# Optimization experiments

Measured on AMD Instinct MI355X. Metric: run time of the kernel, lower is better.

The kernel has to match this reference:

```python
import jax, jax.numpy as jnp
import numpy as np

LAYER_SIZE = 8
STACK_SIZE = 2
RES_CH = 64
SKIP_CH = 128
N = 16
L = 8192
NUM_BLOCKS = LAYER_SIZE * STACK_SIZE


def _dilations():
    return [2 ** lev for _ in range(STACK_SIZE) for lev in range(LAYER_SIZE)]


def setup_inputs() -> dict:
    key = jax.random.key(0)
    k1, k2, k3, k4 = jax.random.split(key, 4)
    x = jax.random.normal(k1, (N, RES_CH, L), dtype=jnp.float32)
    # conv weights scaled ~1/sqrt(fan_in) to keep gates in a sane range
    W_dil = jax.random.normal(k2, (NUM_BLOCKS, RES_CH, RES_CH, 2), dtype=jnp.float32) * 0.088
    W_res = jax.random.normal(k3, (NUM_BLOCKS, RES_CH, RES_CH), dtype=jnp.float32) * 0.125
    W_skip = jax.random.normal(k4, (NUM_BLOCKS, SKIP_CH, RES_CH), dtype=jnp.float32) * 0.125
    return {"x": x, "W_dil": W_dil, "W_res": W_res, "W_skip": W_skip}


def reference(x, W_dil, W_res, W_skip):
    dilations = _dilations()
    out = x
    skips = []
    for i, d in enumerate(dilations):
        wd = W_dil[i]    # (Cout, Cin, 2)
        wr = W_res[i]    # (C, C) 1x1
        ws = W_skip[i]   # (S, C) 1x1
        # dilated causal conv, kernel_size=2, no padding -> length L-d
        y = (jnp.einsum('oi,nil->nol', wd[:, :, 0], out[:, :, :-d])
             + jnp.einsum('oi,nil->nol', wd[:, :, 1], out[:, :, d:]))
        # gated activation: tanh and sigmoid of the SAME dilated output
        g = jnp.tanh(y) * jax.nn.sigmoid(y)
        # NOTE: source has `if self.pooling > 1` with self.pooling a bool,
        # so AvgPool1d is never applied; pool_out == g always.
        res = jnp.einsum('oi,nil->nol', wr, g) + out[:, :, -g.shape[2]:]
        skips.append(jnp.einsum('oi,nil->nol', ws, g))
        out = res
    osize = out.shape[2]
    skip_out = skips[0][:, :, -osize:]
    for s in skips[1:]:
        skip_out = skip_out + s[:, :, -osize:]
    return (out, skip_out)
```

## Files before the change

### kernel.cpp

```cpp
#include <hip/hip_runtime.h>


#define NBATCH 16
#define C 64
#define SC 128
#define L0 8192
#define OSIZE 7682
#define TILE 64
#define ST 128

typedef __bf16 bf16x8 __attribute__((ext_vector_type(8)));
typedef __bf16 bf16x4 __attribute__((ext_vector_type(4)));
typedef float  f32x4  __attribute__((ext_vector_type(4)));

__global__ __launch_bounds__(256) void pack_weights(
    const float* __restrict__ Wd, const float* __restrict__ Wr,
    const float* __restrict__ Ws,
    __bf16* __restrict__ Wdm, __bf16* __restrict__ Wrm, __bf16* __restrict__ Wsm)
{
    int idx = blockIdx.x * 256 + threadIdx.x;
    if (idx < 131072) {
        int kp = idx & 127, o = (idx >> 7) & 63, ly = idx >> 13;
        int k = kp & 63, tap = kp >> 6;
        Wdm[idx] = (__bf16)Wd[(((ly * 64 + o) * 64 + k) << 1) + tap];
    } else if (idx < 196608) {
        int j = idx - 131072;
        Wrm[j] = (__bf16)Wr[j];
    } else if (idx < 327680) {
        int j = idx - 196608;
        Wsm[j] = (__bf16)Ws[j];
    }
}

__global__ __launch_bounds__(256, 2) void wavenet_epoch5(
    const float* __restrict__ src, int Lin,
    float* __restrict__ dst,
    const __bf16* __restrict__ Wdm,
    const __bf16* __restrict__ Wrm,
    __bf16* __restrict__ gst, size_t slotHW)
{
    __shared__ __bf16 sxp[8][112][8];
    __shared__ __bf16 sgp[8][96][8];

    const int Lf = Lin - 31;
    const int n  = blockIdx.y;
    const int o0 = blockIdx.x * 64;
    if (o0 >= Lf) return;

    const int t    = threadIdx.x;
    const int lane = t & 63;
    const int wv   = t >> 6;
    const int q    = lane >> 4;
    const int nn   = lane & 15;
    const int kgw  = 2 * wv + (q >> 1);
    const int hf4  = (q & 1) * 4;

    f32x4 xs[6];
    const float* base = src + (size_t)(n * C + wv * 16 + q * 4) * L0 + o0;
    #pragma unroll
    for (int nt = 0; nt < 6; ++nt) {
        int p = nt * 16 + nn;
        bool inb = (o0 + p) < Lin;
        #pragma unroll
        for (int r = 0; r < 4; ++r)
            xs[nt][r] = inb ? base[(size_t)r * L0 + p] : 0.f;
        bf16x4 v;
        #pragma unroll
        for (int r = 0; r < 4; ++r) v[r] = (__bf16)xs[nt][r];
        *(bf16x4*)(&sxp[0][0][0] + ((size_t)kgw * 112 + 16 + p) * 8 + hf4) = v;
    }
    {
        bf16x4 z = {(__bf16)0.f, (__bf16)0.f, (__bf16)0.f, (__bf16)0.f};
        *(bf16x4*)(&sxp[0][0][0] + ((size_t)kgw * 112 + nn) * 8 + hf4) = z;
    }
    __syncthreads();

    #pragma unroll 1
    for (int l = 0; l < 5; ++l) {
        const int d = 1 << l;

        const __bf16* aw = Wdm + ((size_t)l * 64 + wv * 16 + nn) * 128 + q * 8;
        bf16x8 aW0 = *(const bf16x8*)(aw);
        bf16x8 aW1 = *(const bf16x8*)(aw + 32);
        bf16x8 aW2 = *(const bf16x8*)(aw + 64);
        bf16x8 aW3 = *(const bf16x8*)(aw + 96);
        #pragma unroll
        for (int nt = 0; nt < 6; ++nt) {
            int p = nt * 16 + nn;
            f32x4 acc = {0.f, 0.f, 0.f, 0.f};
            acc = __builtin_amdgcn_mfma_f32_16x16x32_bf16(aW0,
                    *(const bf16x8*)(&sxp[0][0][0] + ((size_t)(q    ) * 112 + 16 + p - d) * 8), acc, 0, 0, 0);
            acc = __builtin_amdgcn_mfma_f32_16x16x32_bf16(aW1,
                    *(const bf16x8*)(&sxp[0][0][0] + ((size_t)(4 + q) * 112 + 16 + p - d) * 8), acc, 0, 0, 0);
            acc = __builtin_amdgcn_mfma_f32_16x16x32_bf16(aW2,
                    *(const bf16x8*)(&sxp[0][0][0] + ((size_t)(q    ) * 112 + 16 + p    ) * 8), acc, 0, 0, 0);
            acc = __builtin_amdgcn_mfma_f32_16x16x32_bf16(aW3,
                    *(const bf16x8*)(&sxp[0][0][0] + ((size_t)(4 + q) * 112 + 16 + p    ) * 8), acc, 0, 0, 0);
            bf16x4 gv;
            #pragma unroll
            for (int r = 0; r < 4; ++r) {
                float y = fminf(fmaxf(acc[r], -20.f), 20.f);
                float u = __expf(y);
                gv[r] = (__bf16)(u * (u - 1.f) / fmaf(u, u, 1.f));
            }
            *(bf16x4*)(&sgp[0][0][0] + ((size_t)kgw * 96 + p) * 8 + hf4) = gv;
        }
        __syncthreads();

        const __bf16* ar = Wrm + ((size_t)l * 64 + wv * 16 + nn) * 64 + q * 8;
        bf16x8 aR0 = *(const bf16x8*)ar;
        bf16x8 aR1 = *(const bf16x8*)(ar + 32);
        #pragma unroll
        for (int nt = 0; nt < 6; ++nt) {
            int p = nt * 16 + nn;
            bf16x8 b0 = *(const bf16x8*)(&sgp[0][0][0] + ((size_t)(q    ) * 96 + p) * 8);
            bf16x8 b1 = *(const bf16x8*)(&sgp[0][0][0] + ((size_t)(4 + q) * 96 + p) * 8);
            xs[nt] = __builtin_amdgcn_mfma_f32_16x16x32_bf16(aR1, b1,
                     __builtin_amdgcn_mfma_f32_16x16x32_bf16(aR0, b0, xs[nt], 0, 0, 0),
                     0, 0, 0);
            bf16x4 v;
            #pragma unroll
            for (int r = 0; r < 4; ++r) v[r] = (__bf16)xs[nt][r];
            *(bf16x4*)(&sxp[0][0][0] + ((size_t)kgw * 112 + 16 + p) * 8 + hf4) = v;
        }

        const int Dl = (2 << l) - 1;
        const int Ll = Lin - Dl;
        const int sb = Ll - OSIZE;
        __bf16* gsl = gst + (size_t)l * slotHW;
        for (int item = t; item < 8 * 64; item += 256) {
            int p  = 31 + (item & 63);
            int kg = item >> 6;
            int i  = o0 + p - Dl;
            if (i >= sb && i < Ll) {
                *(bf16x8*)(gsl + (((size_t)n * 8 + kg) * OSIZE + (i - sb)) * 8)
                    = *(const bf16x8*)(&sgp[0][0][0] + ((size_t)kg * 96 + p) * 8);
            }
        }
        __syncthreads();
    }

    #pragma unroll
    for (int nt = 1; nt < 6; ++nt) {
        int p = nt * 16 + nn;
        if (p >= 31 && p < 95) {
            int i = o0 + p - 31;
            if (i < Lf) {
                #pragma unroll
                for (int r = 0; r < 4; ++r)
                    dst[(size_t)(n * C + wv * 16 + q * 4 + r) * L0 + i] = xs[nt][r];
            }
        }
    }
}

__global__ __launch_bounds__(256) void wavenet_layer_mfma(
    const float* __restrict__ src, int src_stride, int Lin,
    float* __restrict__ dst, int dst_stride,
    const __bf16* __restrict__ Wdm,
    const __bf16* __restrict__ Wrm,
    __bf16* __restrict__ gout,
    int d)
{
    extern __shared__ char smem_raw[];
    const int W    = TILE + d;
    const int Lout = Lin - d;
    const int n  = blockIdx.y;
    const int l0 = blockIdx.x * TILE;
    if (l0 >= Lout) return;
    const int np = min(TILE, Lout - l0);

    __bf16* sxp  = (__bf16*)smem_raw;
    float*  sres = (float*)(smem_raw + (size_t)8 * W * 8 * 2);
    __bf16* sgp  = (__bf16*)(sres + 64 * 65);

    const int t    = threadIdx.x;
    const int lane = t & 63;
    const int wv   = t >> 6;
    const int q    = lane >> 4;
    const int nn   = lane & 15;

    for (int item = t; item < 8 * W; item += 256) {
        int kg = item / W;
        int p  = item % W;
        bool inb = (l0 + p) < Lin;
        const float* col = src + (size_t)(n * C + kg * 8) * src_stride + l0 + p;
        float v[8];
        #pragma unroll
        for (int j = 0; j < 8; ++j) v[j] = inb ? col[(size_t)j * src_stride] : 0.f;
        bf16x8 bv;
        #pragma unroll
        for (int j = 0; j < 8; ++j) bv[j] = (__bf16)v[j];
        *(bf16x8*)(sxp + ((size_t)kg * W + p) * 8) = bv;
        int pr = p - d;
        if (pr >= 0 && pr < TILE) {
            #pragma unroll
            for (int j = 0; j < 8; ++j) sres[(kg * 8 + j) * 65 + pr] = v[j];
        }
    }
    __syncthreads();

    const __bf16* arow = Wdm + (size_t)(wv * 16 + nn) * 128 + q * 8;
    bf16x8 aW[4];
    #pragma unroll
    for (int ks = 0; ks < 4; ++ks) aW[ks] = *(const bf16x8*)(arow + ks * 32);

    #pragma unroll
    for (int nt = 0; nt < 4; ++nt) {
        int p0 = nt * 16;
        f32x4 acc = {0.f, 0.f, 0.f, 0.f};
        acc = __builtin_amdgcn_mfma_f32_16x16x32_bf16(aW[0],
                *(const bf16x8*)(sxp + ((size_t)(q    ) * W + p0 + nn    ) * 8), acc, 0, 0, 0);
        acc = __builtin_amdgcn_mfma_f32_16x16x32_bf16(aW[1],
                *(const bf16x8*)(sxp + ((size_t)(4 + q) * W + p0 + nn    ) * 8), acc, 0, 0, 0);
        acc = __builtin_amdgcn_mfma_f32_16x16x32_bf16(aW[2],
                *(const bf16x8*)(sxp + ((size_t)(q    ) * W + p0 + nn + d) * 8), acc, 0, 0, 0);
        acc = __builtin_amdgcn_mfma_f32_16x16x32_bf16(aW[3],
                *(const bf16x8*)(sxp + ((size_t)(4 + q) * W + p0 + nn + d) * 8), acc, 0, 0, 0);
        bf16x4 gv;
        #pragma unroll
        for (int r = 0; r < 4; ++r) {
            float y = fminf(fmaxf(acc[r], -20.f), 20.f);
            float u = __expf(y);
            gv[r] = (__bf16)(u * (u - 1.f) / fmaf(u, u, 1.f));
        }
        *(bf16x4*)(sgp + ((size_t)(2 * wv + (q >> 1)) * 64 + p0 + nn) * 8 + (q & 1) * 4) = gv;
    }
    __syncthreads();

    const __bf16* rrow = Wrm + (size_t)(wv * 16 + nn) * 64 + q * 8;
    bf16x8 aR0 = *(const bf16x8*)rrow;
    bf16x8 aR1 = *(const bf16x8*)(rrow + 32);
    #pragma unroll
    for (int nt = 0; nt < 4; ++nt) {
        int p0 = nt * 16;
        f32x4 acc = {0.f, 0.f, 0.f, 0.f};
        acc = __builtin_amdgcn_mfma_f32_16x16x32_bf16(aR0,
                *(const bf16x8*)(sgp + ((size_t)(q    ) * 64 + p0 + nn) * 8), acc, 0, 0, 0);
        acc = __builtin_amdgcn_mfma_f32_16x16x32_bf16(aR1,
                *(const bf16x8*)(sgp + ((size_t)(4 + q) * 64 + p0 + nn) * 8), acc, 0, 0, 0);
        if (p0 + nn < np) {
            #pragma unroll
            for (int r = 0; r < 4; ++r) {
                int ch = wv * 16 + q * 4 + r;
                dst[(size_t)(n * C + ch) * dst_stride + l0 + p0 + nn]
                    = acc[r] + sres[ch * 65 + p0 + nn];
            }
        }
    }

    const int sbase = Lout - OSIZE;
    for (int item = t; item < 8 * TILE; item += 256) {
        int p  = item & 63;
        int kg = item >> 6;
        int l  = l0 + p;
        if (l >= sbase && l < Lout) {
            *(bf16x8*)(gout + (((size_t)n * 8 + kg) * OSIZE + (l - sbase)) * 8)
                = *(const bf16x8*)(sgp + ((size_t)kg * 64 + p) * 8);
        }
    }
}

__global__ __launch_bounds__(256, 3) void skip_gemm(
    const __bf16* __restrict__ g,
    const __bf16* __restrict__ Wsm,
    float* __restrict__ skip,
    int G, int lybase, int init)
{
    __shared__ __bf16 Bb[3][8][ST][8];
    const int n  = blockIdx.y;
    const int l0 = blockIdx.x * ST;
    const int t  = threadIdx.x;
    const int lane = t & 63;
    const int wv   = __builtin_amdgcn_readfirstlane(t >> 6);
    const int q = lane >> 4, nn = lane & 15;

    f32x4 acc[2][8];
    #pragma unroll
    for (int mt = 0; mt < 2; ++mt)
        #pragma unroll
        for (int nt = 0; nt < 8; ++nt) acc[mt][nt] = (f32x4){0.f, 0.f, 0.f, 0.f};

    auto stage = [&](int buf, int gi) {
        const __bf16* gl = g + ((size_t)gi * NBATCH + n) * (size_t)8 * OSIZE * 8;
        #pragma unroll
        for (int j = 0; j < 4; ++j) {
            int kg   = 2 * wv + (j >> 1);
            int half = j & 1;
            const __bf16* srcp = gl + ((size_t)kg * OSIZE + l0 + half * 64) * 8
                                    + (size_t)lane * 8;
            __builtin_amdgcn_global_load_lds(
                (const __attribute__((address_space(1))) void*)srcp,
                (__attribute__((address_space(3))) void*)&Bb[buf][kg][half * 64][0],
                16, 0, 0);
        }
    };

    stage(0, 0);
    stage(1, G > 1 ? 1 : 0);

    for (int gi = 0; gi < G; ++gi) {
        const int cur = gi % 3;
        asm volatile("s_waitcnt vmcnt(4)" ::: "memory");
        __builtin_amdgcn_s_barrier();

        const __bf16* Wl = Wsm + (size_t)(lybase + gi) * SC * 64;
        bf16x8 a00 = *(const bf16x8*)(Wl + (size_t)(wv * 32 +      nn) * 64 +  0 + q * 8);
        bf16x8 a01 = *(const bf16x8*)(Wl + (size_t)(wv * 32 +      nn) * 64 + 32 + q * 8);
        bf16x8 a10 = *(const bf16x8*)(Wl + (size_t)(wv * 32 + 16 + nn) * 64 +  0 + q * 8);
        bf16x8 a11 = *(const bf16x8*)(Wl + (size_t)(wv * 32 + 16 + nn) * 64 + 32 + q * 8);
        __builtin_amdgcn_sched_barrier(0);

        stage((gi + 2) % 3, gi + 2 < G ? gi + 2 : G - 1);
        __builtin_amdgcn_sched_barrier(0);

        #pragma unroll
        for (int ks = 0; ks < 2; ++ks) {
            #pragma unroll
            for (int nt = 0; nt < 8; ++nt) {
                bf16x8 b = *(const bf16x8*)&Bb[cur][ks * 4 + q][nt * 16 + nn][0];
                acc[0][nt] = __builtin_amdgcn_mfma_f32_16x16x32_bf16(
                                 ks ? a01 : a00, b, acc[0][nt], 0, 0, 0);
                acc[1][nt] = __builtin_amdgcn_mfma_f32_16x16x32_bf16(
                                 ks ? a11 : a10, b, acc[1][nt], 0, 0, 0);
            }
        }
        __builtin_amdgcn_s_barrier();
    }

    #pragma unroll
    for (int mt = 0; mt < 2; ++mt)
        #pragma unroll
        for (int nt = 0; nt < 8; ++nt) {
            int p = l0 + nt * 16 + nn;
            if (p < OSIZE) {
                #pragma unroll
                for (int r = 0; r < 4; ++r) {
                    int s = wv * 32 + mt * 16 + q * 4 + r;
                    size_t idx = ((size_t)n * SC + s) * OSIZE + p;
                    float v = acc[mt][nt][r];
                    skip[idx] = init ? v : (skip[idx] + v);
                }
            }
        }
}

extern "C" void kernel_launch(void* const* d_in, const int* in_sizes, int n_in,
                              void* d_out, int out_size, void* d_ws, size_t ws_size,
                              hipStream_t stream) {
    const float* x      = (const float*)d_in[0];
    const float* W_dil  = (const float*)d_in[1];
    const float* W_res  = (const float*)d_in[2];
    const float* W_skip = (const float*)d_in[3];

    float* out  = (float*)d_out;
    float* skip = out + (size_t)NBATCH * C * OSIZE;

    float*  bufA = (float*)d_ws;
    float*  bufB = bufA + (size_t)NBATCH * C * L0;
    __bf16* Wdm  = (__bf16*)(bufB + (size_t)NBATCH * C * L0);
    __bf16* Wrm  = Wdm + 16 * 64 * 128;
    __bf16* Wsm  = Wrm + 16 * 64 * 64;
    __bf16* gst  = Wsm + 16 * 128 * 64;

    const size_t slotHW = (size_t)NBATCH * 8 * OSIZE * 8;
    const int G = 8;

    pack_weights<<<1280, 256, 0, stream>>>(W_dil, W_res, W_skip, Wdm, Wrm, Wsm);

    {
        int Lin = L0, Lf = Lin - 31;
        dim3 grid((Lf + 63) / 64, NBATCH);
        wavenet_epoch5<<<grid, 256, 0, stream>>>(
            x, Lin, bufA, Wdm, Wrm, gst, slotHW);
    }
    {
        const float* src = bufA; float* dsts[3] = {bufB, bufA, bufB};
        int Lin = L0 - 31;
        for (int k = 0; k < 3; ++k) {
            int i = 5 + k, d = 32 << k, Lout = Lin - d;
            int W = TILE + d;
            size_t smem = (size_t)128 * W + 64 * 65 * 4 + 8 * 64 * 8 * 2;
            dim3 grid((Lout + TILE - 1) / TILE, NBATCH);
            wavenet_layer_mfma<<<grid, 256, smem, stream>>>(
                src, L0, Lin, dsts[k], L0,
                Wdm + (size_t)i * 64 * 128, Wrm + (size_t)i * 64 * 64,
                gst + (size_t)(i % G) * slotHW, d);
            src = dsts[k]; Lin = Lout;
        }
    }
    {
        dim3 sgrid((OSIZE + ST - 1) / ST, NBATCH);
        skip_gemm<<<sgrid, 256, 0, stream>>>(gst, Wsm, skip, G, 0, 1);
    }

    {
        int Lin = L0 - 255;
        int Lf = Lin - 31;
        dim3 grid((Lf + 63) / 64, NBATCH);
        wavenet_epoch5<<<grid, 256, 0, stream>>>(
            bufB, Lin, bufA,
            Wdm + (size_t)8 * 64 * 128, Wrm + (size_t)8 * 64 * 64,
            gst, slotHW);
    }
    {
        const float* src = bufA;
        int Lin = L0 - 255 - 31;
        float* dsts[3] = {bufB, bufA, out};
        int strides[3] = {L0, L0, OSIZE};
        for (int k = 0; k < 3; ++k) {
            int i = 13 + k, d = 32 << k, Lout = Lin - d;
            int W = TILE + d;
            size_t smem = (size_t)128 * W + 64 * 65 * 4 + 8 * 64 * 8 * 2;
            dim3 grid((Lout + TILE - 1) / TILE, NBATCH);
            wavenet_layer_mfma<<<grid, 256, smem, stream>>>(
                src, L0, Lin, dsts[k], strides[k],
                Wdm + (size_t)i * 64 * 128, Wrm + (size_t)i * 64 * 64,
                gst + (size_t)(i % G) * slotHW, d);
            src = dsts[k]; Lin = Lout;
        }
    }
    {
        dim3 sgrid((OSIZE + ST - 1) / ST, NBATCH);
        skip_gemm<<<sgrid, 256, 0, stream>>>(gst, Wsm, skip, G, 8, 0);
    }
}
```

Measured before the change: 555.4 us.

## Halve skip GEMM tile width and double-buffer weight fragments in registers

```diff
diff --git a/kernel.cpp b/kernel.cpp
--- a/kernel.cpp
+++ b/kernel.cpp
@@ -7,7 +7,7 @@
 #define L0 8192
 #define OSIZE 7682
 #define TILE 64
-#define ST 128
+#define SST 64
 
 typedef __bf16 bf16x8 __attribute__((ext_vector_type(8)));
 typedef __bf16 bf16x4 __attribute__((ext_vector_type(4)));
@@ -261,77 +261,88 @@
     }
 }
 
-__global__ __launch_bounds__(256, 3) void skip_gemm(
+__global__ __launch_bounds__(256, 4) void skip_gemm(
     const __bf16* __restrict__ g,
     const __bf16* __restrict__ Wsm,
     float* __restrict__ skip,
     int G, int lybase, int init)
 {
-    __shared__ __bf16 Bb[3][8][ST][8];
+    __shared__ __bf16 Bb[3][8][SST][8];
     const int n  = blockIdx.y;
-    const int l0 = blockIdx.x * ST;
+    const int l0 = blockIdx.x * SST;
     const int t  = threadIdx.x;
     const int lane = t & 63;
     const int wv   = __builtin_amdgcn_readfirstlane(t >> 6);
     const int q = lane >> 4, nn = lane & 15;
 
-    f32x4 acc[2][8];
+    f32x4 acc[2][4];
     #pragma unroll
     for (int mt = 0; mt < 2; ++mt)
         #pragma unroll
-        for (int nt = 0; nt < 8; ++nt) acc[mt][nt] = (f32x4){0.f, 0.f, 0.f, 0.f};
+        for (int nt = 0; nt < 4; ++nt) acc[mt][nt] = (f32x4){0.f, 0.f, 0.f, 0.f};
 
     auto stage = [&](int buf, int gi) {
         const __bf16* gl = g + ((size_t)gi * NBATCH + n) * (size_t)8 * OSIZE * 8;
         #pragma unroll
-        for (int j = 0; j < 4; ++j) {
-            int kg   = 2 * wv + (j >> 1);
-            int half = j & 1;
-            const __bf16* srcp = gl + ((size_t)kg * OSIZE + l0 + half * 64) * 8
-                                    + (size_t)lane * 8;
+        for (int j = 0; j < 2; ++j) {
+            int kg = 2 * wv + j;
+            const __bf16* srcp = gl + ((size_t)kg * OSIZE + l0) * 8 + (size_t)lane * 8;
             __builtin_amdgcn_global_load_lds(
                 (const __attribute__((address_space(1))) void*)srcp,
-                (__attribute__((address_space(3))) void*)&Bb[buf][kg][half * 64][0],
+                (__attribute__((address_space(3))) void*)&Bb[buf][kg][0][0],
                 16, 0, 0);
         }
     };
-
+    auto loadA = [&](int gi, bf16x8* A) {
+        const __bf16* Wl = Wsm + (size_t)(lybase + gi) * SC * 64;
+        A[0] = *(const bf16x8*)(Wl + (size_t)(wv * 32 +      nn) * 64 +      q * 8);
+        A[1] = *(const bf16x8*)(Wl + (size_t)(wv * 32 +      nn) * 64 + 32 + q * 8);
+        A[2] = *(const bf16x8*)(Wl + (size_t)(wv * 32 + 16 + nn) * 64 +      q * 8);
+        A[3] = *(const bf16x8*)(Wl + (size_t)(wv * 32 + 16 + nn) * 64 + 32 + q * 8);
+    };
+    auto mfma16 = [&](const bf16x8* A, int cur) {
+        #pragma unroll
+        for (int ks = 0; ks < 2; ++ks) {
+            #pragma unroll
+            for (int nt = 0; nt < 4; ++nt) {
+                bf16x8 b = *(const bf16x8*)&Bb[cur][ks * 4 + q][nt * 16 + nn][0];
+                acc[0][nt] = __builtin_amdgcn_mfma_f32_16x16x32_bf16(
+                                 A[ks], b, acc[0][nt], 0, 0, 0);
+                acc[1][nt] = __builtin_amdgcn_mfma_f32_16x16x32_bf16(
+                                 A[2 + ks], b, acc[1][nt], 0, 0, 0);
+            }
+        }
+    };
+
+    bf16x8 aA[4], aB[4];
     stage(0, 0);
+    loadA(0, aA);
     stage(1, G > 1 ? 1 : 0);
 
-    for (int gi = 0; gi < G; ++gi) {
-        const int cur = gi % 3;
-        asm volatile("s_waitcnt vmcnt(4)" ::: "memory");
+    for (int gi = 0; gi < G; gi += 2) {
+        asm volatile("s_waitcnt vmcnt(6)" ::: "memory");
         __builtin_amdgcn_s_barrier();
-
-        const __bf16* Wl = Wsm + (size_t)(lybase + gi) * SC * 64;
-        bf16x8 a00 = *(const bf16x8*)(Wl + (size_t)(wv * 32 +      nn) * 64 +  0 + q * 8);
-        bf16x8 a01 = *(const bf16x8*)(Wl + (size_t)(wv * 32 +      nn) * 64 + 32 + q * 8);
-        bf16x8 a10 = *(const bf16x8*)(Wl + (size_t)(wv * 32 + 16 + nn) * 64 +  0 + q * 8);
-        bf16x8 a11 = *(const bf16x8*)(Wl + (size_t)(wv * 32 + 16 + nn) * 64 + 32 + q * 8);
         __builtin_amdgcn_sched_barrier(0);
-
+        loadA(gi + 1 < G ? gi + 1 : gi, aB);
         stage((gi + 2) % 3, gi + 2 < G ? gi + 2 : G - 1);
         __builtin_amdgcn_sched_barrier(0);
-
-        #pragma unroll
-        for (int ks = 0; ks < 2; ++ks) {
-            #pragma unroll
-            for (int nt = 0; nt < 8; ++nt) {
-                bf16x8 b = *(const bf16x8*)&Bb[cur][ks * 4 + q][nt * 16 + nn][0];
-                acc[0][nt] = __builtin_amdgcn_mfma_f32_16x16x32_bf16(
-                                 ks ? a01 : a00, b, acc[0][nt], 0, 0, 0);
-                acc[1][nt] = __builtin_amdgcn_mfma_f32_16x16x32_bf16(
-                                 ks ? a11 : a10, b, acc[1][nt], 0, 0, 0);
-            }
-        }
+        mfma16(aA, gi % 3);
         __builtin_amdgcn_s_barrier();
+
+        asm volatile("s_waitcnt vmcnt(6)" ::: "memory");
+        __builtin_amdgcn_s_barrier();
+        __builtin_amdgcn_sched_barrier(0);
+        loadA(gi + 2 < G ? gi + 2 : gi, aA);
+        stage((gi + 3) % 3, gi + 3 < G ? gi + 3 : G - 1);
+        __builtin_amdgcn_sched_barrier(0);
+        mfma16(aB, (gi + 1) % 3);
+        __builtin_amdgcn_s_barrier();
     }
 
     #pragma unroll
     for (int mt = 0; mt < 2; ++mt)
         #pragma unroll
-        for (int nt = 0; nt < 8; ++nt) {
+        for (int nt = 0; nt < 4; ++nt) {
             int p = l0 + nt * 16 + nn;
             if (p < OSIZE) {
                 #pragma unroll
@@ -390,7 +401,7 @@
         }
     }
     {
-        dim3 sgrid((OSIZE + ST - 1) / ST, NBATCH);
+        dim3 sgrid((OSIZE + SST - 1) / SST, NBATCH);
         skip_gemm<<<sgrid, 256, 0, stream>>>(gst, Wsm, skip, G, 0, 1);
     }
 
@@ -421,7 +432,7 @@
         }
     }
     {
-        dim3 sgrid((OSIZE + ST - 1) / ST, NBATCH);
+        dim3 sgrid((OSIZE + SST - 1) / SST, NBATCH);
         skip_gemm<<<sgrid, 256, 0, stream>>>(gst, Wsm, skip, G, 8, 0);
     }
 }
```

Result: no change. 553.7 us (-0.3%).
